# Optimization experiments

Hardware: AMD Instinct MI355X
Metric: run time of the kernel (lower is better)

Reference implementation:

```python
import jax, jax.numpy as jnp
import numpy as np

B, N, C, H = 2, 2048, 256, 8
HD = C // H
LN_EPS = 1e-5
BN_EPS = 1e-5  # eval-mode BatchNorm with running_mean=0, running_var=1


def _ln(x, g, b):
    # LayerNorm over last dim
    m = jnp.mean(x, axis=-1, keepdims=True)
    v = jnp.mean((x - m) ** 2, axis=-1, keepdims=True)
    return (x - m) * jax.lax.rsqrt(v + LN_EPS) * g + b


def _ln_cn(x, g, b):
    # x: [B,C,N], normalize over C (torch does transpose -> LN -> transpose)
    return jnp.swapaxes(_ln(jnp.swapaxes(x, 1, 2), g, b), 1, 2)


def _cdist(a, b):
    # a: [B,N,D], b: [B,M,D] -> [B,N,M] euclidean
    d2 = (jnp.sum(a * a, -1)[:, :, None] + jnp.sum(b * b, -1)[:, None, :]
          - 2.0 * jnp.einsum('bnd,bmd->bnm', a, b))
    return jnp.sqrt(jnp.maximum(d2, 0.0))


def _conv1x1(w, x, b=None):
    # w: [O,C], x: [B,C,N]
    y = jnp.einsum('oc,bcn->bon', w, x)
    return y if b is None else y + b[None, :, None]


def setup_inputs() -> dict:
    key = jax.random.key(0)
    ks = jax.random.split(key, 32)
    s = 0.02
    inp = {
        'xyz_A': jax.random.normal(ks[0], (B, N, 3), jnp.float32),
        'featA': jax.random.normal(ks[1], (B, C, N), jnp.float32),
        'xyz_B': jax.random.normal(ks[2], (B, N, 3), jnp.float32),
        'featB': jax.random.normal(ks[3], (B, C, N), jnp.float32),
        'ln_in_g': jnp.ones((C,), jnp.float32),
        'ln_in_b': jnp.zeros((C,), jnp.float32),
        'Wq': jax.random.normal(ks[4], (C, C), jnp.float32) * s,
        'bq': jnp.zeros((C,), jnp.float32),
        'Wk': jax.random.normal(ks[5], (C, C), jnp.float32) * s,
        'bk': jnp.zeros((C,), jnp.float32),
        'Wv': jax.random.normal(ks[6], (C, C), jnp.float32) * s,
        'bv': jnp.zeros((C,), jnp.float32),
        'sb_w1': jax.random.normal(ks[7], (H // 2, 1), jnp.float32) * s,
        'sb_bn_g': jnp.ones((H // 2,), jnp.float32),
        'sb_bn_b': jnp.zeros((H // 2,), jnp.float32),
        'sb_w2': jax.random.normal(ks[8], (H, H // 2), jnp.float32) * s,
        'sb_b2': jnp.zeros((H,), jnp.float32),
        'Wqd': jax.random.normal(ks[9], (C, C), jnp.float32) * s,
        'bqd': jnp.zeros((C,), jnp.float32),
        'Wkd': jax.random.normal(ks[10], (C, C), jnp.float32) * s,
        'bkd': jnp.zeros((C,), jnp.float32),
        'ln_sim_g': jnp.ones((C,), jnp.float32),
        'ln_sim_b': jnp.zeros((C,), jnp.float32),
        'ln_dis_g': jnp.ones((C,), jnp.float32),
        'ln_dis_b': jnp.zeros((C,), jnp.float32),
        'Wf1': jax.random.normal(ks[11], (2 * C, 3 * C), jnp.float32) * s,
        'bnf_g': jnp.ones((2 * C,), jnp.float32),
        'bnf_b': jnp.zeros((2 * C,), jnp.float32),
        'Wf2': jax.random.normal(ks[12], (C, 2 * C), jnp.float32) * s,
        'bf2': jnp.zeros((C,), jnp.float32),
    }
    return inp


def reference(xyz_A, featA, xyz_B, featB, ln_in_g, ln_in_b, Wq, bq, Wk, bk, Wv, bv,
              sb_w1, sb_bn_g, sb_bn_b, sb_w2, sb_b2, Wqd, bqd, Wkd, bkd,
              ln_sim_g, ln_sim_b, ln_dis_g, ln_dis_b, Wf1, bnf_g, bnf_b, Wf2, bf2):
    featA_norm = _ln_cn(featA, ln_in_g, ln_in_b)  # [B,C,N]

    # spatial bias: cdist -> 1x1 conv2d MLP over channel dim
    dist = _cdist(xyz_A, xyz_B)  # [B,N,N]
    h = jnp.einsum('oi,binm->bonm', sb_w1, -dist[:, None])  # [B,H/2,N,N]
    h = h * (sb_bn_g / np.sqrt(1.0 + BN_EPS))[None, :, None, None] + sb_bn_b[None, :, None, None]
    h = jax.nn.relu(h)
    spatial_bias = jnp.einsum('oi,binm->bonm', sb_w2, h) + sb_b2[None, :, None, None]  # [B,H,N,N]

    # similarity path
    q = _conv1x1(Wq, featA_norm, bq).reshape(B, H, HD, N).transpose(0, 1, 3, 2)  # [B,H,N,hd]
    k = _conv1x1(Wk, featB, bk).reshape(B, H, HD, N).transpose(0, 1, 3, 2)
    sim_scores = jnp.einsum('bhnd,bhmd->bhnm', q, k) / np.sqrt(HD) + spatial_bias

    # dissimilarity path: feature-space cdist
    qd = jnp.swapaxes(_conv1x1(Wqd, featA_norm, bqd), 1, 2)  # [B,N,C]
    kd = jnp.swapaxes(_conv1x1(Wkd, featB, bkd), 1, 2)
    dissim_scores = _cdist(qd, kd)[:, None] + spatial_bias  # [B,H,N,N]

    sim_w = jax.nn.softmax(sim_scores, axis=-1)
    dis_w = jax.nn.softmax(dissim_scores, axis=-1)

    v = _conv1x1(Wv, featB, bv).reshape(B, H, HD, N).transpose(0, 1, 3, 2)  # [B,H,N,hd]
    ctx_sim = jnp.einsum('bhnm,bhmd->bhnd', sim_w, v).transpose(0, 1, 3, 2).reshape(B, C, N)
    ctx_sim = _ln_cn(ctx_sim, ln_sim_g, ln_sim_b)
    ctx_dis = jnp.einsum('bhnm,bhmd->bhnd', dis_w, v).transpose(0, 1, 3, 2).reshape(B, C, N)
    ctx_dis = _ln_cn(ctx_dis, ln_dis_g, ln_dis_b)

    fused_in = jnp.concatenate([featA_norm, ctx_sim, ctx_dis], axis=1)  # [B,3C,N]
    f = jnp.einsum('oc,bcn->bon', Wf1, fused_in)
    f = f * (bnf_g / np.sqrt(1.0 + BN_EPS))[None, :, None] + bnf_b[None, :, None]
    f = jax.nn.relu(f)
    fused = jnp.einsum('oc,bcn->bon', Wf2, f) + bf2[None, :, None]

    return fused + featA  # residual (in_channel == out_channel -> Identity)
```

## Files before the change

kernel.cpp:

```cpp
#include <hip/hip_runtime.h>
#include <math.h>

#define B_ 2
#define N_ 2048
#define C_ 256
#define H_ 8
#define HD_ 32
constexpr float LN_EPS_ = 1e-5f;
constexpr float BN_EPS_ = 1e-5f;
constexpr float LOG2E_ = 1.4426950408889634f;
constexpr float ISDL_ = 0.17677669529663687f * 1.4426950408889634f;

typedef __attribute__((ext_vector_type(8))) short bf16x8;
typedef __attribute__((ext_vector_type(4))) float f32x4;

static __device__ inline ushort f2bf(float x) {
    union { float f; uint u; } c{x};
    uint r = (c.u + 0x7FFF + ((c.u >> 16) & 1)) >> 16;
    return (ushort)r;
}
static __device__ inline float bf2f(ushort u) {
    union { uint i; float f; } c; c.i = ((uint)u) << 16; return c.f;
}
static __device__ inline float lane_bcast(float v, int srclane) {
    return __int_as_float(__builtin_amdgcn_ds_bpermute(srclane * 4, __float_as_int(v)));
}
static __device__ inline uint pack_bf2(float lo, float hi) {
    uint ul = __float_as_uint(lo) + 0x8000u;
    uint uh = __float_as_uint(hi) + 0x8000u;
    return __builtin_amdgcn_perm(uh, ul, 0x07060302u);
}

__global__ __launch_bounds__(256)
void k_wconv(const float* __restrict__ Wq, const float* __restrict__ Wk,
             const float* __restrict__ Wv, const float* __restrict__ Wqd,
             const float* __restrict__ Wkd, const float* __restrict__ Wf1,
             const float* __restrict__ Wf2, ushort* __restrict__ dst)
{
    size_t e0 = ((size_t)blockIdx.x * 256 + threadIdx.x) * 8;
    const float* src = Wq; size_t base = 0;
    if (e0 >= 65536)  { src = Wk;  base = 65536; }
    if (e0 >= 131072) { src = Wv;  base = 131072; }
    if (e0 >= 196608) { src = Wqd; base = 196608; }
    if (e0 >= 262144) { src = Wkd; base = 262144; }
    if (e0 >= 327680) { src = Wf1; base = 327680; }
    if (e0 >= 720896) { src = Wf2; base = 720896; }
    float4 a = *(const float4*)(src + (e0 - base));
    float4 b = *(const float4*)(src + (e0 - base) + 4);
    ushort o[8] = {f2bf(a.x), f2bf(a.y), f2bf(a.z), f2bf(a.w),
                   f2bf(b.x), f2bf(b.y), f2bf(b.z), f2bf(b.w)};
    *(uint4*)(dst + e0) = *(uint4*)o;
}

template<bool DO_LN>
__global__ __launch_bounds__(256)
void k_ln_transpose(const float* __restrict__ x,
                    const float* __restrict__ g,
                    const float* __restrict__ bt,
                    ushort* __restrict__ out, int ld)
{
    __shared__ float tile[C_][65];
    __shared__ float red_s[4][64];
    __shared__ float red_q[4][64];
    __shared__ float ms[64];
    __shared__ float rs[64];

    const int b  = blockIdx.x / (N_ / 64);
    const int n0 = (blockIdx.x % (N_ / 64)) * 64;
    const int tid = threadIdx.x;

    for (int i = 0; i < 64; ++i) {
        int c = i * 4 + (tid >> 6);
        int n = tid & 63;
        tile[c][n] = x[((size_t)b * C_ + c) * N_ + n0 + n];
    }
    __syncthreads();

    float gv = 0.f, bv = 0.f;
    if (DO_LN) { gv = g[tid]; bv = bt[tid]; }

    if (DO_LN) {
        const int nl = tid & 63, part = tid >> 6;
        float s = 0.f, q = 0.f;
        for (int j = 0; j < 64; ++j) {
            float v = tile[part * 64 + j][nl];
            s += v; q += v * v;
        }
        red_s[part][nl] = s; red_q[part][nl] = q;
        __syncthreads();
        if (tid < 64) {
            float ss = red_s[0][tid] + red_s[1][tid] + red_s[2][tid] + red_s[3][tid];
            float qq = red_q[0][tid] + red_q[1][tid] + red_q[2][tid] + red_q[3][tid];
            float mean = ss * (1.0f / C_);
            float var  = qq * (1.0f / C_) - mean * mean;
            ms[tid] = mean;
            rs[tid] = rsqrtf(var + LN_EPS_);
        }
        __syncthreads();
    }

    for (int i = 0; i < 64; ++i) {
        float v = tile[tid][i];
        if (DO_LN) v = (v - ms[i]) * rs[i] * gv + bv;
        out[((size_t)b * N_ + n0 + i) * ld + tid] = f2bf(v);
    }
}

template<int EPI, int OUT>
__global__ __launch_bounds__(256)
void k_gemm_bf(const ushort* __restrict__ A, int lda, size_t sAz,
               const ushort* __restrict__ Bw, int ldb, size_t sBz,
               void* __restrict__ Cout_, int ldc, size_t sCz,
               int K,
               const float* __restrict__ aux1,
               const float* __restrict__ aux2)
{
    const int z = blockIdx.z;
    A  += (size_t)z * sAz;
    Bw += (size_t)z * sBz;

    const int r0 = blockIdx.x * 64;
    const int c0 = blockIdx.y * 64;
    const int tid = threadIdx.x;
    const int w = tid >> 6, lane = tid & 63;
    const int wr = w >> 1, wc = w & 1;
    const int ql = lane & 15, g = lane >> 4;

    __shared__ ushort As[64][40];
    __shared__ ushort Bs[64][40];

    f32x4 acc[2][2] = {};
    const int srow = tid >> 2;
    const int sk   = (tid & 3) * 8;

    for (int k0 = 0; k0 < K; k0 += 32) {
        bf16x8 av = *(const bf16x8*)&A[(size_t)(r0 + srow) * lda + k0 + sk];
        bf16x8 bv = *(const bf16x8*)&Bw[(size_t)(c0 + srow) * ldb + k0 + sk];
        __syncthreads();
        *(bf16x8*)&As[srow][sk] = av;
        *(bf16x8*)&Bs[srow][sk] = bv;
        __syncthreads();
        bf16x8 af[2], bf[2];
        #pragma unroll
        for (int i = 0; i < 2; ++i) {
            af[i] = *(const bf16x8*)&As[wr * 32 + i * 16 + ql][8 * g];
            bf[i] = *(const bf16x8*)&Bs[wc * 32 + i * 16 + ql][8 * g];
        }
        #pragma unroll
        for (int mi = 0; mi < 2; ++mi)
            #pragma unroll
            for (int ni = 0; ni < 2; ++ni)
                acc[mi][ni] = __builtin_amdgcn_mfma_f32_16x16x32_bf16(af[mi], bf[ni], acc[mi][ni], 0, 0, 0);
    }

    const float inv_bn = rsqrtf(1.0f + BN_EPS_);
    float*  Cf = (float*)Cout_  + (size_t)z * sCz;
    ushort* Cb = (ushort*)Cout_ + (size_t)z * sCz;
    #pragma unroll
    for (int mi = 0; mi < 2; ++mi) {
        #pragma unroll
        for (int ni = 0; ni < 2; ++ni) {
            #pragma unroll
            for (int r = 0; r < 4; ++r) {
                int row = r0 + wr * 32 + mi * 16 + 4 * g + r;
                int col = c0 + wc * 32 + ni * 16 + ql;
                float v = acc[mi][ni][r];
                if (EPI == 0) {
                    v += aux1[col];
                } else if (EPI == 1) {
                    float qnv = aux1[(size_t)z * N_ + row];
                    float knv = aux2[(size_t)z * N_ + col];
                    v = sqrtf(fmaxf(qnv + knv - 2.0f * v, 0.f));
                } else if (EPI == 2) {
                    v = fmaxf(v * (aux1[col] * inv_bn) + aux2[col], 0.f);
                } else if (EPI == 3) {
                    v += aux1[row];
                }
                if (OUT == 0) Cf[(size_t)row * ldc + col] = v;
                else          Cb[(size_t)row * ldc + col] = f2bf(v);
            }
        }
    }
}

__global__ __launch_bounds__(256)
void k_rownorm(const ushort* __restrict__ x, float* __restrict__ outn)
{
    const int r = blockIdx.x * 4 + (threadIdx.x >> 6);
    const int lane = threadIdx.x & 63;
    uint2 pv = *(const uint2*)&x[(size_t)r * C_ + lane * 4];
    float v0 = bf2f((ushort)(pv.x & 0xffff)), v1 = bf2f((ushort)(pv.x >> 16));
    float v2 = bf2f((ushort)(pv.y & 0xffff)), v3 = bf2f((ushort)(pv.y >> 16));
    float s = v0 * v0 + v1 * v1 + v2 * v2 + v3 * v3;
    #pragma unroll
    for (int off = 32; off; off >>= 1) s += __shfl_xor(s, off);
    if (lane == 0) outn[r] = s;
}

__global__ __launch_bounds__(256)
void k_ln_rows(const float* __restrict__ x, const float* __restrict__ g,
               const float* __restrict__ bt, ushort* __restrict__ outp, int ld)
{
    const int r = blockIdx.x * 4 + (threadIdx.x >> 6);
    const int lane = threadIdx.x & 63;
    float v[4]; float s = 0.f, q = 0.f;
    #pragma unroll
    for (int i = 0; i < 4; ++i) {
        v[i] = x[(size_t)r * C_ + lane + 64 * i];
        s += v[i]; q += v[i] * v[i];
    }
    #pragma unroll
    for (int off = 32; off; off >>= 1) { s += __shfl_xor(s, off); q += __shfl_xor(q, off); }
    float mean = s * (1.0f / C_);
    float var  = q * (1.0f / C_) - mean * mean;
    float rstd = rsqrtf(var + LN_EPS_);
    #pragma unroll
    for (int i = 0; i < 4; ++i) {
        int c = lane + 64 * i;
        outp[(size_t)r * ld + c] = f2bf((v[i] - mean) * rstd * g[c] + bt[c]);
    }
}

__global__ __launch_bounds__(1024, 4)
void k_attn3(const ushort* __restrict__ q_bf,
             const ushort* __restrict__ k_bf,
             const ushort* __restrict__ v_c,
             const float* __restrict__ xyzA,
             const float* __restrict__ xyzB,
             const float* __restrict__ cd,
             const float* __restrict__ sb_w1, const float* __restrict__ sb_bn_g,
             const float* __restrict__ sb_bn_b, const float* __restrict__ sb_w2,
             const float* __restrict__ sb_b2,
             float* __restrict__ ctx_sim, float* __restrict__ ctx_dis)
{
    __shared__ ushort biasL[8][16][72];
    __shared__ float  cds[16][68];
    __shared__ ushort ps[16][16][72];
    __shared__ float  w2Ls[8][4];
    __shared__ float  b2Ls[8];

    const int n0 = blockIdx.x * 16;
    const int b  = blockIdx.y;
    const size_t bN = (size_t)b * N_;
    const int tid = threadIdx.x;
    const int w = tid >> 6, lane = tid & 63;
    const int path = w >> 3, h = w & 7;
    const int ql = lane & 15, g = lane >> 4;

    if (tid < 8) {
        b2Ls[tid] = sb_b2[tid] * LOG2E_;
        #pragma unroll
        for (int i = 0; i < 4; ++i) w2Ls[tid][i] = sb_w2[tid * 4 + i] * LOG2E_;
    }

    const float inv_bn = rsqrtf(1.0f + BN_EPS_);
    float w1s_[4], bnb_[4];
    #pragma unroll
    for (int i = 0; i < 4; ++i) {
        w1s_[i] = sb_w1[i] * sb_bn_g[i] * inv_bn;
        bnb_[i] = sb_bn_b[i];
    }

    const int hgrp = tid >> 9;
    const int t2 = tid & 511;
    const int cq = t2 >> 5, cm2 = t2 & 31;
    const float ax = xyzA[(bN + n0 + cq) * 3 + 0];
    const float ay = xyzA[(bN + n0 + cq) * 3 + 1];
    const float az = xyzA[(bN + n0 + cq) * 3 + 2];

    bf16x8 qfrag = {};
    if (path == 0)
        qfrag = *(const bf16x8*)&q_bf[(bN + n0 + ql) * C_ + h * 32 + 8 * g];

    float m_i = -INFINITY, l_i = 0.f;
    f32x4 ctx0 = {0.f, 0.f, 0.f, 0.f};
    f32x4 ctx1 = {0.f, 0.f, 0.f, 0.f};
    const f32x4 zf = {0.f, 0.f, 0.f, 0.f};

    for (int t = 0; t < N_ / 64; ++t) {
        const int m0 = t * 64;
        __syncthreads();

        {
            const int mA = m0 + 2 * cm2;
            const float* pb = xyzB + (bN + mA) * 3;
            float bx0 = pb[0], by0 = pb[1], bz0 = pb[2];
            float bx1 = pb[3], by1 = pb[4], bz1 = pb[5];
            float dx0 = ax - bx0, dy0 = ay - by0, dz0 = az - bz0;
            float dx1 = ax - bx1, dy1 = ay - by1, dz1 = az - bz1;
            float d0 = sqrtf(dx0 * dx0 + dy0 * dy0 + dz0 * dz0);
            float d1 = sqrtf(dx1 * dx1 + dy1 * dy1 + dz1 * dz1);
            float f0[4], f1[4];
            #pragma unroll
            for (int i = 0; i < 4; ++i) {
                f0[i] = fmaxf(fmaf(-w1s_[i], d0, bnb_[i]), 0.f);
                f1[i] = fmaxf(fmaf(-w1s_[i], d1, bnb_[i]), 0.f);
            }
            #pragma unroll
            for (int hh = 0; hh < 4; ++hh) {
                const int hI = hgrp * 4 + hh;
                const f32x4 w2v = *(const f32x4*)w2Ls[hI];
                float b0 = b2Ls[hI], b1 = b2Ls[hI];
                #pragma unroll
                for (int i = 0; i < 4; ++i) {
                    b0 = fmaf(w2v[i], f0[i], b0);
                    b1 = fmaf(w2v[i], f1[i], b1);
                }
                *(uint*)&biasL[hI][cq][2 * cm2] = pack_bf2(b0, b1);
            }
            if (hgrp) {
                float2 cv = *(const float2*)&cd[(bN + n0 + cq) * (size_t)N_ + mA];
                cds[cq][2 * cm2]     = cv.x * LOG2E_;
                cds[cq][2 * cm2 + 1] = cv.y * LOG2E_;
            }
        }
        __syncthreads();

        bf16x8 af[4];
        if (path == 0) {
            #pragma unroll
            for (int mt = 0; mt < 4; ++mt)
                af[mt] = *(const bf16x8*)&k_bf[(bN + m0 + mt * 16 + ql) * C_ + h * 32 + 8 * g];
        }
        bf16x8 vb[2][2];
        #pragma unroll
        for (int kb = 0; kb < 2; ++kb)
            #pragma unroll
            for (int dt = 0; dt < 2; ++dt)
                vb[kb][dt] = *(const bf16x8*)&v_c[((size_t)b * C_ + h * 32 + dt * 16 + ql) * N_ + m0 + kb * 32 + 8 * g];

        float s[16];
        #pragma unroll
        for (int mt = 0; mt < 4; ++mt) {
            uint2 bw = *(const uint2*)&biasL[h][ql][16 * mt + 4 * g];
            s[4 * mt + 0] = __uint_as_float(bw.x << 16);
            s[4 * mt + 1] = __uint_as_float(bw.x & 0xffff0000u);
            s[4 * mt + 2] = __uint_as_float(bw.y << 16);
            s[4 * mt + 3] = __uint_as_float(bw.y & 0xffff0000u);
        }

        if (path == 0) {
            #pragma unroll
            for (int mt = 0; mt < 4; ++mt) {
                f32x4 sf = __builtin_amdgcn_mfma_f32_16x16x32_bf16(af[mt], qfrag, zf, 0, 0, 0);
                #pragma unroll
                for (int r = 0; r < 4; ++r)
                    s[4 * mt + r] = fmaf(sf[r], ISDL_, s[4 * mt + r]);
            }
        } else {
            #pragma unroll
            for (int mt = 0; mt < 4; ++mt) {
                f32x4 cv = *(const f32x4*)&cds[ql][16 * mt + 4 * g];
                #pragma unroll
                for (int r = 0; r < 4; ++r)
                    s[4 * mt + r] += cv[r];
            }
        }

        float tmax = s[0];
        #pragma unroll
        for (int j = 1; j < 16; ++j) tmax = fmaxf(tmax, s[j]);
        tmax = fmaxf(tmax, __shfl_xor(tmax, 16));
        tmax = fmaxf(tmax, __shfl_xor(tmax, 32));
        if (!__all(tmax <= m_i + 8.0f)) {
            float mnew = fmaxf(m_i, tmax);
            float scl = exp2f(m_i - mnew);
            l_i *= scl;
            #pragma unroll
            for (int r = 0; r < 4; ++r) {
                float sr = lane_bcast(scl, 4 * g + r);
                ctx0[r] *= sr; ctx1[r] *= sr;
            }
            m_i = mnew;
        }
        float lsum = 0.f;
        #pragma unroll
        for (int j = 0; j < 16; ++j) {
            float pj = exp2f(s[j] - m_i);
            s[j] = pj;
            lsum += pj;
        }
        lsum += __shfl_xor(lsum, 16);
        lsum += __shfl_xor(lsum, 32);
        l_i += lsum;

        #pragma unroll
        for (int mt = 0; mt < 4; ++mt) {
            uint2 pk;
            pk.x = pack_bf2(s[4 * mt + 0], s[4 * mt + 1]);
            pk.y = pack_bf2(s[4 * mt + 2], s[4 * mt + 3]);
            *(uint2*)&ps[w][ql][16 * mt + 4 * g] = pk;
        }

        #pragma unroll
        for (int kb = 0; kb < 2; ++kb) {
            bf16x8 pa = *(const bf16x8*)&ps[w][ql][kb * 32 + 8 * g];
            ctx0 = __builtin_amdgcn_mfma_f32_16x16x32_bf16(pa, vb[kb][0], ctx0, 0, 0, 0);
            ctx1 = __builtin_amdgcn_mfma_f32_16x16x32_bf16(pa, vb[kb][1], ctx1, 0, 0, 0);
        }
    }

    float il = 1.0f / l_i;
    float* outp = (path == 0) ? ctx_sim : ctx_dis;
    #pragma unroll
    for (int r = 0; r < 4; ++r) {
        float ir = lane_bcast(il, 4 * g + r);
        size_t base = (bN + n0 + 4 * g + r) * C_ + h * 32;
        outp[base + ql]      = ctx0[r] * ir;
        outp[base + 16 + ql] = ctx1[r] * ir;
    }
}

__global__ __launch_bounds__(256)
void k_transpose_add(const float* __restrict__ fused_t,
                     const float* __restrict__ featA,
                     float* __restrict__ out)
{
    __shared__ float t[64][65];
    const int n0 = blockIdx.x * 64, c0 = blockIdx.y * 64, b = blockIdx.z;
    const int tid = threadIdx.x;
    #pragma unroll
    for (int i = 0; i < 16; ++i) {
        int e = i * 256 + tid;
        int nn = e >> 6, cc = e & 63;
        t[nn][cc] = fused_t[((size_t)b * N_ + n0 + nn) * C_ + c0 + cc];
    }
    __syncthreads();
    #pragma unroll
    for (int i = 0; i < 16; ++i) {
        int e = i * 256 + tid;
        int cc = e >> 6, nn = e & 63;
        size_t idx = ((size_t)b * C_ + c0 + cc) * N_ + n0 + nn;
        out[idx] = t[nn][cc] + featA[idx];
    }
}

extern "C" void kernel_launch(void* const* d_in, const int* in_sizes, int n_in,
                              void* d_out, int out_size, void* d_ws, size_t ws_size,
                              hipStream_t stream)
{
    const float* xyz_A   = (const float*)d_in[0];
    const float* featA   = (const float*)d_in[1];
    const float* xyz_B   = (const float*)d_in[2];
    const float* featB   = (const float*)d_in[3];
    const float* ln_in_g = (const float*)d_in[4];
    const float* ln_in_b = (const float*)d_in[5];
    const float* Wq  = (const float*)d_in[6];
    const float* bq  = (const float*)d_in[7];
    const float* Wk  = (const float*)d_in[8];
    const float* bk  = (const float*)d_in[9];
    const float* Wv  = (const float*)d_in[10];
    const float* bv  = (const float*)d_in[11];
    const float* sb_w1   = (const float*)d_in[12];
    const float* sb_bn_g = (const float*)d_in[13];
    const float* sb_bn_b = (const float*)d_in[14];
    const float* sb_w2   = (const float*)d_in[15];
    const float* sb_b2   = (const float*)d_in[16];
    const float* Wqd = (const float*)d_in[17];
    const float* bqd = (const float*)d_in[18];
    const float* Wkd = (const float*)d_in[19];
    const float* bkd = (const float*)d_in[20];
    const float* ln_sim_g = (const float*)d_in[21];
    const float* ln_sim_b = (const float*)d_in[22];
    const float* ln_dis_g = (const float*)d_in[23];
    const float* ln_dis_b = (const float*)d_in[24];
    const float* Wf1   = (const float*)d_in[25];
    const float* bnf_g = (const float*)d_in[26];
    const float* bnf_b = (const float*)d_in[27];
    const float* Wf2   = (const float*)d_in[28];
    const float* bf2   = (const float*)d_in[29];
    float* out = (float*)d_out;

    float* ws = (float*)d_ws;
    size_t off = 0;
    auto alloc = [&](size_t n) { float* p = ws + off; off += n; return p; };
    const size_t RN = (size_t)B_ * N_;

    ushort* fused_bf = (ushort*)alloc(RN * 384);
    ushort* featB_bf = (ushort*)alloc(RN * 128);
    ushort* q_bf     = (ushort*)alloc(RN * 128);
    ushort* k_bf     = (ushort*)alloc(RN * 128);
    ushort* v_bf     = (ushort*)alloc(RN * 128);
    float*  qdkd     = alloc(RN * 256);
    ushort* qd_bf    = (ushort*)qdkd;
    ushort* kd_bf    = qd_bf + RN * C_;
    ushort* wbf      = (ushort*)alloc(425984);
    float*  qn       = alloc(RN);
    float*  kn       = alloc(RN);
    float*  cd       = alloc((size_t)B_ * N_ * N_);
    float*  ctx_dis_t = alloc(RN * C_);

    float*  ctx_sim_t = qdkd;
    ushort* fh        = (ushort*)cd;
    float*  fused_t   = cd + RN * 256;

    ushort* wq_bf  = wbf;
    ushort* wk_bf  = wbf + 65536;
    ushort* wv_bf  = wbf + 131072;
    ushort* wqd_bf = wbf + 196608;
    ushort* wkd_bf = wbf + 262144;
    ushort* wf1_bf = wbf + 327680;
    ushort* wf2_bf = wbf + 720896;
    (void)ws_size; (void)in_sizes; (void)n_in; (void)out_size;

    dim3 blk(256);

    k_wconv<<<dim3(416), blk, 0, stream>>>(Wq, Wk, Wv, Wqd, Wkd, Wf1, Wf2, wbf);
    k_ln_transpose<true ><<<dim3(B_ * (N_ / 64)), blk, 0, stream>>>(featA, ln_in_g, ln_in_b, fused_bf, 3 * C_);
    k_ln_transpose<false><<<dim3(B_ * (N_ / 64)), blk, 0, stream>>>(featB, nullptr, nullptr, featB_bf, C_);

    k_gemm_bf<0,1><<<dim3(RN / 64, C_ / 64, 1), blk, 0, stream>>>(fused_bf, 3 * C_, 0, wq_bf,  C_, 0, q_bf,  C_, 0, C_, bq,  nullptr);
    k_gemm_bf<0,1><<<dim3(RN / 64, C_ / 64, 1), blk, 0, stream>>>(featB_bf, C_,     0, wk_bf,  C_, 0, k_bf,  C_, 0, C_, bk,  nullptr);
    k_gemm_bf<3,1><<<dim3(C_ / 64, N_ / 64, B_), blk, 0, stream>>>(wv_bf, C_, 0, featB_bf, C_, (size_t)N_ * C_, v_bf, N_, (size_t)C_ * N_, C_, bv, nullptr);
    k_gemm_bf<0,1><<<dim3(RN / 64, C_ / 64, 1), blk, 0, stream>>>(fused_bf, 3 * C_, 0, wqd_bf, C_, 0, qd_bf, C_, 0, C_, bqd, nullptr);
    k_gemm_bf<0,1><<<dim3(RN / 64, C_ / 64, 1), blk, 0, stream>>>(featB_bf, C_,     0, wkd_bf, C_, 0, kd_bf, C_, 0, C_, bkd, nullptr);

    k_rownorm<<<dim3(RN / 4), blk, 0, stream>>>(qd_bf, qn);
    k_rownorm<<<dim3(RN / 4), blk, 0, stream>>>(kd_bf, kn);
    k_gemm_bf<1,0><<<dim3(N_ / 64, N_ / 64, B_), blk, 0, stream>>>(qd_bf, C_, (size_t)N_ * C_,
                                                                   kd_bf, C_, (size_t)N_ * C_,
                                                                   cd, N_, (size_t)N_ * N_, B_ ? C_ : C_, qn, kn);

    k_attn3<<<dim3(N_ / 16, B_), dim3(1024), 0, stream>>>(q_bf, k_bf, v_bf, xyz_A, xyz_B, cd,
                                                          sb_w1, sb_bn_g, sb_bn_b, sb_w2, sb_b2,
                                                          ctx_sim_t, ctx_dis_t);

    k_ln_rows<<<dim3(RN / 4), blk, 0, stream>>>(ctx_sim_t, ln_sim_g, ln_sim_b, fused_bf + C_,     3 * C_);
    k_ln_rows<<<dim3(RN / 4), blk, 0, stream>>>(ctx_dis_t, ln_dis_g, ln_dis_b, fused_bf + 2 * C_, 3 * C_);

    k_gemm_bf<2,1><<<dim3(RN / 64, (2 * C_) / 64, 1), blk, 0, stream>>>(fused_bf, 3 * C_, 0, wf1_bf, 3 * C_, 0, fh, 2 * C_, 0, 3 * C_, bnf_g, bnf_b);
    k_gemm_bf<0,0><<<dim3(RN / 64, C_ / 64, 1), blk, 0, stream>>>(fh, 2 * C_, 0, wf2_bf, 2 * C_, 0, fused_t, C_, 0, 2 * C_, bf2, nullptr);

    k_transpose_add<<<dim3(N_ / 64, C_ / 64, B_), blk, 0, stream>>>(fused_t, featA, out);
}
```

Measured before the change: 234.2 us.

## Split attention key range across two blocks and merge partial softmax results

```diff
diff --git a/kernel.cpp b/kernel.cpp
--- a/kernel.cpp
+++ b/kernel.cpp
@@ -221,8 +221,8 @@
     }
 }
 
-__global__ __launch_bounds__(1024, 4)
-void k_attn3(const ushort* __restrict__ q_bf,
+__global__ __launch_bounds__(1024, 8)
+void k_attn4(const ushort* __restrict__ q_bf,
              const ushort* __restrict__ k_bf,
              const ushort* __restrict__ v_c,
              const float* __restrict__ xyzA,
@@ -231,7 +231,8 @@
              const float* __restrict__ sb_w1, const float* __restrict__ sb_bn_g,
              const float* __restrict__ sb_bn_b, const float* __restrict__ sb_w2,
              const float* __restrict__ sb_b2,
-             float* __restrict__ ctx_sim, float* __restrict__ ctx_dis)
+             ushort* __restrict__ pc,
+             float* __restrict__ pml)
 {
     __shared__ ushort biasL[8][16][72];
     __shared__ float  cds[16][68];
@@ -241,6 +242,7 @@
 
     const int n0 = blockIdx.x * 16;
     const int b  = blockIdx.y;
+    const int half = blockIdx.z;
     const size_t bN = (size_t)b * N_;
     const int tid = threadIdx.x;
     const int w = tid >> 6, lane = tid & 63;
@@ -277,7 +279,10 @@
     f32x4 ctx1 = {0.f, 0.f, 0.f, 0.f};
     const f32x4 zf = {0.f, 0.f, 0.f, 0.f};
 
-    for (int t = 0; t < N_ / 64; ++t) {
+    const int tBeg = half * (N_ / 128);
+    const int tEnd = tBeg + (N_ / 128);
+
+    for (int t = tBeg; t < tEnd; ++t) {
         const int m0 = t * 64;
         __syncthreads();
 
@@ -400,15 +405,39 @@
         }
     }
 
-    float il = 1.0f / l_i;
+    const size_t sl = (size_t)(half * 2 + path) * (B_ * N_);
+    #pragma unroll
+    for (int r = 0; r < 4; ++r) {
+        size_t base = (sl + bN + n0 + 4 * g + r) * C_ + h * 32;
+        pc[base + ql]      = f2bf(ctx0[r]);
+        pc[base + 16 + ql] = f2bf(ctx1[r]);
+    }
+    if (g == 0) {
+        size_t mlb = ((sl + bN + n0 + ql) * H_ + h) * 2;
+        pml[mlb]     = m_i;
+        pml[mlb + 1] = l_i;
+    }
+}
+
+__global__ __launch_bounds__(256)
+void k_merge(const ushort* __restrict__ pc, const float* __restrict__ pml,
+             float* __restrict__ ctx_sim, float* __restrict__ ctx_dis)
+{
+    const int row = blockIdx.x;
+    const int path = blockIdx.y;
+    const int c = threadIdx.x;
+    const int h = c >> 5;
+    const size_t i0 = (size_t)(0 * 2 + path) * (B_ * N_) + row;
+    const size_t i1 = (size_t)(1 * 2 + path) * (B_ * N_) + row;
+    const float m0 = pml[(i0 * H_ + h) * 2], l0 = pml[(i0 * H_ + h) * 2 + 1];
+    const float m1 = pml[(i1 * H_ + h) * 2], l1 = pml[(i1 * H_ + h) * 2 + 1];
+    const float M = fmaxf(m0, m1);
+    const float w0 = exp2f(m0 - M), w1 = exp2f(m1 - M);
+    const float il = 1.0f / fmaf(l0, w0, l1 * w1);
+    const float v0 = bf2f(pc[i0 * C_ + c]);
+    const float v1 = bf2f(pc[i1 * C_ + c]);
     float* outp = (path == 0) ? ctx_sim : ctx_dis;
-    #pragma unroll
-    for (int r = 0; r < 4; ++r) {
-        float ir = lane_bcast(il, 4 * g + r);
-        size_t base = (bN + n0 + 4 * g + r) * C_ + h * 32;
-        outp[base + ql]      = ctx0[r] * ir;
-        outp[base + 16 + ql] = ctx1[r] * ir;
-    }
+    outp[(size_t)row * C_ + c] = fmaf(v0, w0, v1 * w1) * il;
 }
 
 __global__ __launch_bounds__(256)
@@ -489,6 +518,8 @@
     float*  kn       = alloc(RN);
     float*  cd       = alloc((size_t)B_ * N_ * N_);
     float*  ctx_dis_t = alloc(RN * C_);
+    ushort* pc       = (ushort*)alloc(4 * RN * C_ / 2);
+    float*  pml      = alloc(4 * RN * H_ * 2);
 
     float*  ctx_sim_t = qdkd;
     ushort* fh        = (ushort*)cd;
@@ -519,11 +550,12 @@
     k_rownorm<<<dim3(RN / 4), blk, 0, stream>>>(kd_bf, kn);
     k_gemm_bf<1,0><<<dim3(N_ / 64, N_ / 64, B_), blk, 0, stream>>>(qd_bf, C_, (size_t)N_ * C_,
                                                                    kd_bf, C_, (size_t)N_ * C_,
-                                                                   cd, N_, (size_t)N_ * N_, B_ ? C_ : C_, qn, kn);
-
-    k_attn3<<<dim3(N_ / 16, B_), dim3(1024), 0, stream>>>(q_bf, k_bf, v_bf, xyz_A, xyz_B, cd,
-                                                          sb_w1, sb_bn_g, sb_bn_b, sb_w2, sb_b2,
-                                                          ctx_sim_t, ctx_dis_t);
+                                                                   cd, N_, (size_t)N_ * N_, C_, qn, kn);
+
+    k_attn4<<<dim3(N_ / 16, B_, 2), dim3(1024), 0, stream>>>(q_bf, k_bf, v_bf, xyz_A, xyz_B, cd,
+                                                             sb_w1, sb_bn_g, sb_bn_b, sb_w2, sb_b2,
+                                                             pc, pml);
+    k_merge<<<dim3(RN, 2), blk, 0, stream>>>(pc, pml, ctx_sim_t, ctx_dis_t);
 
     k_ln_rows<<<dim3(RN / 4), blk, 0, stream>>>(ctx_sim_t, ln_sim_g, ln_sim_b, fused_bf + C_,     3 * C_);
     k_ln_rows<<<dim3(RN / 4), blk, 0, stream>>>(ctx_dis_t, ln_dis_g, ln_dis_b, fused_bf + 2 * C_, 3 * C_);
```

Result: slower. 541.5 us (+131.2%).
